# Kernel optimization log

Measured on AMD Instinct MI355X. Metric: run time of the kernel, lower is better.

The kernel has to match this reference:

```python
import jax, jax.numpy as jnp
import numpy as np

E = 1024  # hidden_size
H = 16    # num_heads
D = E // H  # head_dim
LN_EPS = 1e-5


def setup_inputs() -> dict:
    key = jax.random.key(0)
    ks = jax.random.split(key, 7)
    B, S = 4, 2048
    scale = 1.0 / np.sqrt(E)
    return {
        "txt_emb": jax.random.normal(ks[0], (B, S, E), dtype=jnp.float32),
        "in_proj_w": jax.random.normal(ks[1], (3 * E, E), dtype=jnp.float32) * scale,
        "in_proj_b": jnp.zeros((3 * E,), dtype=jnp.float32),
        "out_proj_w": jax.random.normal(ks[2], (E, E), dtype=jnp.float32) * scale,
        "out_proj_b": jnp.zeros((E,), dtype=jnp.float32),
        "ln_gamma": jnp.ones((E,), dtype=jnp.float32),
        "ln_beta": jnp.zeros((E,), dtype=jnp.float32),
    }


def _layer_norm(x, gamma, beta):
    mu = jnp.mean(x, axis=-1, keepdims=True)
    var = jnp.var(x, axis=-1, keepdims=True)
    return (x - mu) * jax.lax.rsqrt(var + LN_EPS) * gamma + beta


def reference(txt_emb, in_proj_w, in_proj_b, out_proj_w, out_proj_b, ln_gamma, ln_beta):
    B, S, _ = txt_emb.shape
    # joint QKV projection (torch nn.MultiheadAttention semantics: x @ W.T + b)
    qkv = jnp.einsum('bse,fe->bsf', txt_emb, in_proj_w) + in_proj_b  # [B,S,3E]
    q, k, v = jnp.split(qkv, 3, axis=-1)
    # [B,H,S,D]
    q = q.reshape(B, S, H, D).transpose(0, 2, 1, 3)
    k = k.reshape(B, S, H, D).transpose(0, 2, 1, 3)
    v = v.reshape(B, S, H, D).transpose(0, 2, 1, 3)
    scores = jnp.einsum('bhqd,bhkd->bhqk', q, k) / np.sqrt(D)  # [B,H,S,S]
    causal = jnp.tril(jnp.ones((S, S), dtype=bool))
    scores = jnp.where(causal, scores, jnp.float32(-jnp.inf))
    attn = jax.nn.softmax(scores, axis=-1)
    ctx = jnp.einsum('bhqk,bhkd->bhqd', attn, v)  # [B,H,S,D]
    ctx = ctx.transpose(0, 2, 1, 3).reshape(B, S, E)
    attn_out = jnp.einsum('bse,fe->bsf', ctx, out_proj_w) + out_proj_b
    return _layer_norm(txt_emb + attn_out, ln_gamma, ln_beta)
```

## Files before the change

kernel.cpp:

```cpp
#include <hip/hip_runtime.h>
#include <hip/hip_bf16.h>
#include <stdint.h>

#define B_   4
#define S_   2048
#define E_   1024
#define H_   16
#define D_   64
#define M_   (B_ * S_)
#define E3_  (3 * E_)

#define QSCALE 0.18033688011112042f

typedef __bf16 bf16_t;
typedef bf16_t bf16x8 __attribute__((ext_vector_type(8)));
typedef float  f32x4  __attribute__((ext_vector_type(4)));
typedef float  f32x16 __attribute__((ext_vector_type(16)));

__device__ __forceinline__ ushort f2bf(float f) {
  union { float f; uint32_t u; } v; v.f = f;
  uint32_t r = v.u + 0x7fffu + ((v.u >> 16) & 1u);
  return (ushort)(r >> 16);
}

__device__ __forceinline__ unsigned cvtpk(float lo, float hi_) {
  unsigned d;
  asm("v_cvt_pk_bf16_f32 %0, %1, %2" : "=v"(d) : "v"(lo), "v"(hi_));
  return d;
}

__device__ __forceinline__ void gload_lds16(const void* g, void* l) {
  __builtin_amdgcn_global_load_lds((const __attribute__((address_space(1))) void*)g,
                                   (__attribute__((address_space(3))) void*)l,
                                   16, 0, 0);
}

__global__ __launch_bounds__(256) void cvt_f32_bf16(const float* __restrict__ in,
                                                    ushort* __restrict__ out, int n4,
                                                    int scale_row4, float scale) {
  int i = blockIdx.x * blockDim.x + threadIdx.x;
  if (i < n4) {
    float4 v = reinterpret_cast<const float4*>(in)[i];
    if (i < scale_row4) { v.x *= scale; v.y *= scale; v.z *= scale; v.w *= scale; }
    ushort4 o;
    o.x = f2bf(v.x); o.y = f2bf(v.y); o.z = f2bf(v.z); o.w = f2bf(v.w);
    reinterpret_cast<ushort4*>(out)[i] = o;
  }
}

__global__ __launch_bounds__(512) void gemm_qkv_8ph(const ushort* __restrict__ A,
                                                    const ushort* __restrict__ Bt,
                                                    const float* __restrict__ bias,
                                                    ushort* __restrict__ qkout,
                                                    ushort* __restrict__ vTout) {
  __shared__ __align__(16) char lds[3][49152];

  const int tid = threadIdx.x;
  const int lane = tid & 63, wid = tid >> 6;
  const int wr = wid >> 2, wc = wid & 3;

  const int b0 = blockIdx.x;
  const int nb = (b0 & 7) * 96 + (b0 >> 3);
  const int bm = (nb / 12) * 128;
  const int bn = (nb % 12) * 256;

  const int l8 = lane >> 3;
  const int sw = (lane & 7) ^ l8;
  const ushort* aS = A  + (size_t)(bm + wid * 16 + l8) * 1024 + sw * 8;
  const ushort* bS = Bt + (size_t)(bn + wid * 32 + l8) * 1024 + sw * 8;

#define STAGE_A(T, BUF, J) \
  gload_lds16(aS + (size_t)(T) * 64 + (J) * 8 * 1024, (void*)((BUF) + (wid * 2 + (J)) * 1024))
#define STAGE_B(T, BUF, J) \
  gload_lds16(bS + (size_t)(T) * 64 + (J) * 8 * 1024, (void*)((BUF) + 16384 + (wid * 4 + (J)) * 1024))

  const int lr15 = lane & 15;
  const int ksub = lane >> 4;
  const int slot0 = ((ksub + 0) ^ (lr15 & 7)) * 16;
  const int slot1 = ((ksub + 4) ^ (lr15 & 7)) * 16;
  const int arow_b = (wr * 64 + lr15) * 128;
  const int brow_b = (wc * 64 + lr15) * 128;

#define LDA_ALL(BUF)                                                              \
  do {                                                                            \
    _Pragma("unroll")                                                             \
    for (int m = 0; m < 4; ++m) {                                                 \
      af[m][0] = *(const bf16x8*)((BUF) + arow_b + m * 2048 + slot0);             \
      af[m][1] = *(const bf16x8*)((BUF) + arow_b + m * 2048 + slot1);             \
    }                                                                             \
  } while (0)
#define LDB2(BUF, NB)                                                             \
  do {                                                                            \
    _Pragma("unroll")                                                             \
    for (int n = 0; n < 2; ++n) {                                                 \
      bfr[n][0] = *(const bf16x8*)((BUF) + 16384 + brow_b + ((NB) + n) * 2048 + slot0); \
      bfr[n][1] = *(const bf16x8*)((BUF) + 16384 + brow_b + ((NB) + n) * 2048 + slot1); \
    }                                                                             \
  } while (0)
#define MFMA16(NB)                                                                \
  do {                                                                            \
    __builtin_amdgcn_s_setprio(1);                                                \
    _Pragma("unroll")                                                             \
    for (int m = 0; m < 4; ++m)                                                   \
      _Pragma("unroll")                                                           \
      for (int n = 0; n < 2; ++n)                                                 \
        _Pragma("unroll")                                                         \
        for (int kh = 0; kh < 2; ++kh)                                            \
          acc[m][(NB) + n] = __builtin_amdgcn_mfma_f32_16x16x32_bf16(             \
              af[m][kh], bfr[n][kh], acc[m][(NB) + n], 0, 0, 0);                  \
    __builtin_amdgcn_s_setprio(0);                                                \
  } while (0)

  f32x4 acc[4][4] = {};
  bf16x8 af[4][2], bfr[2][2];

  char* buf0 = &lds[0][0];
  char* buf1 = &lds[1][0];
  char* buf2 = &lds[2][0];

  STAGE_A(0, buf0, 0); STAGE_A(0, buf0, 1);
  STAGE_B(0, buf0, 0); STAGE_B(0, buf0, 1); STAGE_B(0, buf0, 2); STAGE_B(0, buf0, 3);
  STAGE_A(1, buf1, 0); STAGE_A(1, buf1, 1);
  STAGE_B(1, buf1, 0); STAGE_B(1, buf1, 1); STAGE_B(1, buf1, 2); STAGE_B(1, buf1, 3);
  asm volatile("s_waitcnt vmcnt(6)" ::: "memory");
  __builtin_amdgcn_s_barrier();
  __builtin_amdgcn_sched_barrier(0);

  for (int t = 0; t < 16; ++t) {
    if (t < 14) { STAGE_A(t + 2, buf2, 0); STAGE_A(t + 2, buf2, 1); STAGE_B(t + 2, buf2, 0); }
    LDA_ALL(buf0);
    LDB2(buf0, 0);
    __builtin_amdgcn_s_barrier();
    asm volatile("s_waitcnt lgkmcnt(0)" ::: "memory");
    __builtin_amdgcn_sched_barrier(0);
    MFMA16(0);
    __builtin_amdgcn_s_barrier();
    __builtin_amdgcn_sched_barrier(0);
    if (t < 14) { STAGE_B(t + 2, buf2, 1); STAGE_B(t + 2, buf2, 2); STAGE_B(t + 2, buf2, 3); }
    LDB2(buf0, 2);
    __builtin_amdgcn_s_barrier();
    asm volatile("s_waitcnt lgkmcnt(0)" ::: "memory");
    __builtin_amdgcn_sched_barrier(0);
    MFMA16(2);
    if (t < 14) asm volatile("s_waitcnt vmcnt(6)" ::: "memory");
    else if (t == 14) asm volatile("s_waitcnt vmcnt(0)" ::: "memory");
    __builtin_amdgcn_s_barrier();
    __builtin_amdgcn_sched_barrier(0);
    char* tmp = buf0; buf0 = buf1; buf1 = buf2; buf2 = tmp;
  }

#pragma unroll
  for (int m = 0; m < 4; ++m) {
#pragma unroll
    for (int n = 0; n < 4; ++n) {
      const int col = bn + wc * 64 + n * 16 + lr15;
      float bv = bias[col];
      if (col < 1024) bv *= QSCALE;
      const int row0 = bm + wr * 64 + m * 16 + ksub * 4;
      if (col < 2048) {
#pragma unroll
        for (int r = 0; r < 4; ++r)
          qkout[(size_t)(row0 + r) * 2048 + col] = f2bf(acc[m][n][r] + bv);
      } else {
        ushort4 vv;
        vv.x = f2bf(acc[m][n][0] + bv);
        vv.y = f2bf(acc[m][n][1] + bv);
        vv.z = f2bf(acc[m][n][2] + bv);
        vv.w = f2bf(acc[m][n][3] + bv);
        const size_t vidx = ((size_t)((row0 >> 11) * 1024 + (col - 2048))) * 2048 + (row0 & 2047);
        *reinterpret_cast<ushort4*>(&vTout[vidx]) = vv;
      }
    }
  }
#undef STAGE_A
#undef STAGE_B
#undef LDA_ALL
#undef LDB2
#undef MFMA16
}

__global__ __launch_bounds__(256) void gemm_bt0(const ushort* __restrict__ A,
                                                const ushort* __restrict__ Bt,
                                                const float* __restrict__ bias,
                                                float* __restrict__ out0,
                                                int Mdim, int Ndim, int K) {
  __shared__ __align__(16) ushort As[128 * 32];
  __shared__ __align__(16) ushort Bs[128 * 32];

  const int tid  = threadIdx.x;
  const int lane = tid & 63, wid = tid >> 6;
  const int wr = wid >> 1, wc = wid & 1;

  const int nx = gridDim.x;
  const int nwg = nx * gridDim.y;
  const int b0 = blockIdx.y * nx + blockIdx.x;
  const int nb = (b0 & 7) * (nwg >> 3) + (b0 >> 3);
  const int bm = (nb / nx) * 128, bn = (nb % nx) * 128;

  const int lrow = lane & 15, lk8 = (lane >> 4) * 8, lg4 = (lane >> 4) * 4;
  const int srow = tid >> 2;
  const int skk  = (tid & 3) * 8;

  f32x4 acc[4][4] = {};

  for (int k0 = 0; k0 < K; k0 += 32) {
#pragma unroll
    for (int j = 0; j < 2; ++j) {
      const ushort* ga = A  + (size_t)(bm + j * 64 + srow) * K + k0 + skk;
      const ushort* gb = Bt + (size_t)(bn + j * 64 + srow) * K + k0 + skk;
      gload_lds16(ga, (void*)&As[(j * 256 + wid * 64) * 8]);
      gload_lds16(gb, (void*)&Bs[(j * 256 + wid * 64) * 8]);
    }
    __syncthreads();

    bf16x8 af[4], bfv[4];
#pragma unroll
    for (int rb = 0; rb < 4; ++rb)
      af[rb] = *reinterpret_cast<const bf16x8*>(&As[(wr * 64 + rb * 16 + lrow) * 32 + lk8]);
#pragma unroll
    for (int cb = 0; cb < 4; ++cb)
      bfv[cb] = *reinterpret_cast<const bf16x8*>(&Bs[(wc * 64 + cb * 16 + lrow) * 32 + lk8]);
#pragma unroll
    for (int rb = 0; rb < 4; ++rb)
#pragma unroll
      for (int cb = 0; cb < 4; ++cb)
        acc[rb][cb] = __builtin_amdgcn_mfma_f32_16x16x32_bf16(af[rb], bfv[cb], acc[rb][cb], 0, 0, 0);
    __syncthreads();
  }

#pragma unroll
  for (int rb = 0; rb < 4; ++rb) {
#pragma unroll
    for (int cb = 0; cb < 4; ++cb) {
      const int col = bn + wc * 64 + cb * 16 + lrow;
      const float bv = bias[col];
      const int row0 = bm + wr * 64 + rb * 16 + lg4;
#pragma unroll
      for (int r = 0; r < 4; ++r)
        out0[(size_t)(row0 + r) * Ndim + col] = acc[rb][cb][r] + bv;
    }
  }
}

__global__ __launch_bounds__(512) void attn_causal(const ushort* __restrict__ qk,
                                                   const ushort* __restrict__ vT,
                                                   ushort* __restrict__ ctx) {
  __shared__ __align__(16) char lds[2][16384];

  const int tid = threadIdx.x;
  const int w = tid >> 6, lane = tid & 63;
  const int l31 = lane & 31, hi = lane >> 5;

  const int bid = blockIdx.x;
  const int bh = (bid & 7) * 8 + ((bid >> 3) & 7);
  const int g6 = bid >> 6;
  const int qb = (g6 < 4) ? (7 - g6) : (g6 - 4);
  const int b = bh >> 4, h = bh & 15;
  const int qbase = qb * 256;
  const int tmax = 4 * qb + 3;
  const int qw = qbase + w * 32;
  const int q_g = qw + l31;
  const int my_tmax = (qw + 31) >> 6;

  const ushort* qrow = qk + (size_t)(b * S_ + q_g) * 2048 + h * 64;
  bf16x8 qf[4];
#pragma unroll
  for (int st = 0; st < 4; ++st)
    qf[st] = *reinterpret_cast<const bf16x8*>(qrow + st * 16 + hi * 8);

  const int srow = tid >> 3;
  const int swz  = ((tid & 7) * 16) ^ ((srow & 7) << 4);
  const char* kbase = (const char*)qk + ((size_t)(b * S_ + srow) * 2048 + 1024 + h * 64) * 2 + swz;
  const char* vbase = (const char*)vT + ((size_t)(bh * 64 + srow) * 2048) * 2 + swz;

  f32x16 Ot0 = {}, Ot1 = {};
  float m_r = -__builtin_inff(), l_r = 0.f;

  const int kswz = ((l31 & 7) << 4);

#define STAGE(T, BUFI)                                                              \
  do {                                                                              \
    gload_lds16(kbase + (size_t)(T) * (64 * 2048 * 2), &lds[BUFI][w * 1024]);       \
    gload_lds16(vbase + (size_t)(T) * 128,             &lds[BUFI][8192 + w * 1024]);\
  } while (0)

  STAGE(0, 0);
  for (int t = 0; t <= tmax; ++t) {
    const int bufi = t & 1;
    if (t < tmax) {
      STAGE(t + 1, bufi ^ 1);
      asm volatile("s_waitcnt vmcnt(2)" ::: "memory");
    } else {
      asm volatile("s_waitcnt vmcnt(0)" ::: "memory");
    }
    __builtin_amdgcn_s_barrier();
    __builtin_amdgcn_sched_barrier(0);

    if (t <= my_tmax) {
      const char* Kt = &lds[bufi][0];
      const char* Vp = &lds[bufi][8192];

      f32x16 T0 = {}, T1 = {};
#pragma unroll
      for (int st = 0; st < 4; ++st) {
        const int cb = (st * 32 + hi * 16) ^ kswz;
        bf16x8 k0 = *(const bf16x8*)(Kt + l31 * 128 + cb);
        bf16x8 k1 = *(const bf16x8*)(Kt + (32 + l31) * 128 + cb);
        T0 = __builtin_amdgcn_mfma_f32_32x32x16_bf16(k0, qf[st], T0, 0, 0, 0);
        T1 = __builtin_amdgcn_mfma_f32_32x32x16_bf16(k1, qf[st], T1, 0, 0, 0);
      }

      float p[32];
      const bool needmask = (t * 64 + 63) > qw;
      const int kvb = t * 64 + 4 * hi;
#pragma unroll
      for (int g = 0; g < 4; ++g) {
#pragma unroll
        for (int j = 0; j < 4; ++j) {
          float v0 = T0[4 * g + j], v1 = T1[4 * g + j];
          if (needmask) {
            const int kv0 = kvb + 8 * g + j;
            v0 = (kv0      <= q_g) ? v0 : -__builtin_inff();
            v1 = (kv0 + 32 <= q_g) ? v1 : -__builtin_inff();
          }
          p[4 * g + j] = v0;
          p[16 + 4 * g + j] = v1;
        }
      }
      float pmax = p[0];
#pragma unroll
      for (int i = 1; i < 31; i += 2) pmax = fmaxf(fmaxf(pmax, p[i]), p[i + 1]);
      pmax = fmaxf(pmax, p[31]);
      pmax = fmaxf(pmax, __shfl_xor(pmax, 32));

      if (!__all(pmax - m_r <= 8.f)) {
        const float mn = fmaxf(m_r, pmax);
        const float sc = exp2f(m_r - mn);
        m_r = mn;
        l_r *= sc;
#pragma unroll
        for (int i = 0; i < 16; ++i) { Ot0[i] *= sc; Ot1[i] *= sc; }
      }
      float sum = 0.f;
#pragma unroll
      for (int i = 0; i < 32; ++i) { p[i] = exp2f(p[i] - m_r); sum += p[i]; }
      sum += __shfl_xor(sum, 32);
      l_r += sum;

#pragma unroll
      for (int ks = 0; ks < 4; ++ks) {
        const unsigned a = cvtpk(p[8 * ks + 0], p[8 * ks + 1]);
        const unsigned bq = cvtpk(p[8 * ks + 2], p[8 * ks + 3]);
        const unsigned c = cvtpk(p[8 * ks + 4], p[8 * ks + 5]);
        const unsigned d = cvtpk(p[8 * ks + 6], p[8 * ks + 7]);
        const unsigned x = hi ? a : c;
        const unsigned y = hi ? bq : d;
        const unsigned xp = (unsigned)__shfl_xor((int)x, 32);
        const unsigned yp = (unsigned)__shfl_xor((int)y, 32);
        union { unsigned u[4]; bf16x8 v; } pa;
        pa.u[0] = hi ? xp : a;
        pa.u[1] = hi ? yp : bq;
        pa.u[2] = hi ? c : xp;
        pa.u[3] = hi ? d : yp;
        const int cb = (ks * 32 + hi * 16) ^ kswz;
        bf16x8 v0 = *(const bf16x8*)(Vp + l31 * 128 + cb);
        bf16x8 v1 = *(const bf16x8*)(Vp + (32 + l31) * 128 + cb);
        Ot0 = __builtin_amdgcn_mfma_f32_32x32x16_bf16(v0, pa.v, Ot0, 0, 0, 0);
        Ot1 = __builtin_amdgcn_mfma_f32_32x32x16_bf16(v1, pa.v, Ot1, 0, 0, 0);
      }
    }
    __builtin_amdgcn_s_barrier();
    __builtin_amdgcn_sched_barrier(0);
  }

  const float inv = 1.0f / l_r;
  ushort* crow = ctx + (size_t)(b * S_ + q_g) * 1024 + h * 64;
#pragma unroll
  for (int g = 0; g < 4; ++g) {
#pragma unroll
    for (int jp = 0; jp < 2; ++jp) {
      const int d0 = 2 * jp + 8 * g + 4 * hi;
      const int r = 4 * g + 2 * jp;
      *(unsigned*)(crow + d0)      = cvtpk(Ot0[r] * inv, Ot0[r + 1] * inv);
      *(unsigned*)(crow + 32 + d0) = cvtpk(Ot1[r] * inv, Ot1[r + 1] * inv);
    }
  }
#undef STAGE
}

__global__ __launch_bounds__(256) void resid_ln(const float* __restrict__ x,
                                                const float* __restrict__ ao,
                                                const float* __restrict__ gamma,
                                                const float* __restrict__ beta,
                                                float* __restrict__ out) {
  const int row = blockIdx.x;
  const int tid = threadIdx.x;
  const size_t base = (size_t)row * E_;

  float4 xv = reinterpret_cast<const float4*>(x + base)[tid];
  float4 av = reinterpret_cast<const float4*>(ao + base)[tid];
  const float v0 = xv.x + av.x, v1 = xv.y + av.y, v2 = xv.z + av.z, v3 = xv.w + av.w;
  float s  = v0 + v1 + v2 + v3;
  float s2 = v0 * v0 + v1 * v1 + v2 * v2 + v3 * v3;
#pragma unroll
  for (int off = 32; off >= 1; off >>= 1) {
    s  += __shfl_xor(s, off);
    s2 += __shfl_xor(s2, off);
  }
  __shared__ float red[8];
  const int wid = tid >> 6, lane = tid & 63;
  if (lane == 0) { red[wid] = s; red[4 + wid] = s2; }
  __syncthreads();
  s  = red[0] + red[1] + red[2] + red[3];
  s2 = red[4] + red[5] + red[6] + red[7];
  const float mu  = s * (1.f / E_);
  const float var = s2 * (1.f / E_) - mu * mu;
  const float rsd = rsqrtf(var + 1e-5f);

  float4 gv = reinterpret_cast<const float4*>(gamma)[tid];
  float4 bv = reinterpret_cast<const float4*>(beta)[tid];
  float4 ov;
  ov.x = (v0 - mu) * rsd * gv.x + bv.x;
  ov.y = (v1 - mu) * rsd * gv.y + bv.y;
  ov.z = (v2 - mu) * rsd * gv.z + bv.z;
  ov.w = (v3 - mu) * rsd * gv.w + bv.w;
  reinterpret_cast<float4*>(out + base)[tid] = ov;
}

extern "C" void kernel_launch(void* const* d_in, const int* in_sizes, int n_in,
                              void* d_out, int out_size, void* d_ws, size_t ws_size,
                              hipStream_t stream) {
  (void)in_sizes; (void)n_in; (void)out_size; (void)ws_size;
  const float* x     = (const float*)d_in[0];
  const float* w_in  = (const float*)d_in[1];
  const float* b_in  = (const float*)d_in[2];
  const float* w_out = (const float*)d_in[3];
  const float* b_out = (const float*)d_in[4];
  const float* gamma = (const float*)d_in[5];
  const float* beta  = (const float*)d_in[6];
  float* out = (float*)d_out;

  char* ws = (char*)d_ws;
  ushort* xb    = (ushort*)(ws);
  ushort* winb  = (ushort*)(ws + 16777216);
  ushort* woutb = (ushort*)(ws + 23068672);
  ushort* qkb   = (ushort*)(ws + 25165824);
  ushort* vTb   = (ushort*)(ws + 58720256);
  ushort* ctxb  = (ushort*)(ws + 75497472);
  float*  ao    = (float*)(ws + 92274688);

  cvt_f32_bf16<<<dim3((M_ * E_) / 4 / 256), 256, 0, stream>>>(x, xb, (M_ * E_) / 4, 0, 1.f);
  cvt_f32_bf16<<<dim3((E3_ * E_) / 4 / 256), 256, 0, stream>>>(w_in, winb, (E3_ * E_) / 4,
                                                               (E_ * E_) / 4, QSCALE);
  cvt_f32_bf16<<<dim3((E_ * E_) / 4 / 256), 256, 0, stream>>>(w_out, woutb, (E_ * E_) / 4, 0, 1.f);

  gemm_qkv_8ph<<<dim3(768), 512, 0, stream>>>(xb, winb, b_in, qkb, vTb);
  attn_causal<<<dim3(512), 512, 0, stream>>>(qkb, vTb, ctxb);
  gemm_bt0<<<dim3(E_ / 128, M_ / 128), 256, 0, stream>>>(ctxb, woutb, b_out, ao, M_, E_, E_);
  resid_ln<<<dim3(M_), 256, 0, stream>>>(x, ao, gamma, beta, out);
}
```

Measured before the change: 212.0 us.

## Pipeline output projection GEMM with triple-buffered LDS and rebalance causal attention rows

Replaces the simple single-buffered output-projection GEMM with a 512-thread, 128x256-tile kernel. It uses a three-stage LDS ring with staggered async global-to-LDS loads, swizzled LDS layout and MFMA priority hints, modeled on the existing QKV GEMM. This is meant to hide global load latency and cut barrier stalls. Separately, the causal attention kernel now assigns each workgroup interleaved query strips across the whole sequence, so every block does a similar amount of causal work instead of whole 256-row query blocks of very different length. This adds a larger LDS footprint per block, fewer GEMM workgroups, and longer KV loops per attention block.

```diff
diff --git a/kernel.cpp b/kernel.cpp
--- a/kernel.cpp
+++ b/kernel.cpp
@@ -179,67 +179,123 @@
 #undef MFMA16
 }
 
-__global__ __launch_bounds__(256) void gemm_bt0(const ushort* __restrict__ A,
-                                                const ushort* __restrict__ Bt,
-                                                const float* __restrict__ bias,
-                                                float* __restrict__ out0,
-                                                int Mdim, int Ndim, int K) {
-  __shared__ __align__(16) ushort As[128 * 32];
-  __shared__ __align__(16) ushort Bs[128 * 32];
-
-  const int tid  = threadIdx.x;
+__global__ __launch_bounds__(512) void gemm_out_8ph(const ushort* __restrict__ A,
+                                                    const ushort* __restrict__ Bt,
+                                                    const float* __restrict__ bias,
+                                                    float* __restrict__ out0) {
+  __shared__ __align__(16) char lds[3][49152];
+
+  const int tid = threadIdx.x;
   const int lane = tid & 63, wid = tid >> 6;
-  const int wr = wid >> 1, wc = wid & 1;
-
-  const int nx = gridDim.x;
-  const int nwg = nx * gridDim.y;
-  const int b0 = blockIdx.y * nx + blockIdx.x;
-  const int nb = (b0 & 7) * (nwg >> 3) + (b0 >> 3);
-  const int bm = (nb / nx) * 128, bn = (nb % nx) * 128;
-
-  const int lrow = lane & 15, lk8 = (lane >> 4) * 8, lg4 = (lane >> 4) * 4;
-  const int srow = tid >> 2;
-  const int skk  = (tid & 3) * 8;
+  const int wr = wid >> 2, wc = wid & 3;
+
+  const int b0 = blockIdx.x;
+  const int nb = (b0 & 7) * 32 + (b0 >> 3);
+  const int bm = (nb >> 2) * 128;
+  const int bn = (nb & 3) * 256;
+
+  const int l8 = lane >> 3;
+  const int sw = (lane & 7) ^ l8;
+  const ushort* aS = A  + (size_t)(bm + wid * 16 + l8) * 1024 + sw * 8;
+  const ushort* bS = Bt + (size_t)(bn + wid * 32 + l8) * 1024 + sw * 8;
+
+#define STAGE_A(T, BUF, J) \
+  gload_lds16(aS + (size_t)(T) * 64 + (J) * 8 * 1024, (void*)((BUF) + (wid * 2 + (J)) * 1024))
+#define STAGE_B(T, BUF, J) \
+  gload_lds16(bS + (size_t)(T) * 64 + (J) * 8 * 1024, (void*)((BUF) + 16384 + (wid * 4 + (J)) * 1024))
+
+  const int lr15 = lane & 15;
+  const int ksub = lane >> 4;
+  const int slot0 = ((ksub + 0) ^ (lr15 & 7)) * 16;
+  const int slot1 = ((ksub + 4) ^ (lr15 & 7)) * 16;
+  const int arow_b = (wr * 64 + lr15) * 128;
+  const int brow_b = (wc * 64 + lr15) * 128;
+
+#define LDA_ALL(BUF)                                                              \
+  do {                                                                            \
+    _Pragma("unroll")                                                             \
+    for (int m = 0; m < 4; ++m) {                                                 \
+      af[m][0] = *(const bf16x8*)((BUF) + arow_b + m * 2048 + slot0);             \
+      af[m][1] = *(const bf16x8*)((BUF) + arow_b + m * 2048 + slot1);             \
+    }                                                                             \
+  } while (0)
+#define LDB2(BUF, NB)                                                             \
+  do {                                                                            \
+    _Pragma("unroll")                                                             \
+    for (int n = 0; n < 2; ++n) {                                                 \
+      bfr[n][0] = *(const bf16x8*)((BUF) + 16384 + brow_b + ((NB) + n) * 2048 + slot0); \
+      bfr[n][1] = *(const bf16x8*)((BUF) + 16384 + brow_b + ((NB) + n) * 2048 + slot1); \
+    }                                                                             \
+  } while (0)
+#define MFMA16(NB)                                                                \
+  do {                                                                            \
+    __builtin_amdgcn_s_setprio(1);                                                \
+    _Pragma("unroll")                                                             \
+    for (int m = 0; m < 4; ++m)                                                   \
+      _Pragma("unroll")                                                           \
+      for (int n = 0; n < 2; ++n)                                                 \
+        _Pragma("unroll")                                                         \
+        for (int kh = 0; kh < 2; ++kh)                                            \
+          acc[m][(NB) + n] = __builtin_amdgcn_mfma_f32_16x16x32_bf16(             \
+              af[m][kh], bfr[n][kh], acc[m][(NB) + n], 0, 0, 0);                  \
+    __builtin_amdgcn_s_setprio(0);                                                \
+  } while (0)
 
   f32x4 acc[4][4] = {};
-
-  for (int k0 = 0; k0 < K; k0 += 32) {
-#pragma unroll
-    for (int j = 0; j < 2; ++j) {
-      const ushort* ga = A  + (size_t)(bm + j * 64 + srow) * K + k0 + skk;
-      const ushort* gb = Bt + (size_t)(bn + j * 64 + srow) * K + k0 + skk;
-      gload_lds16(ga, (void*)&As[(j * 256 + wid * 64) * 8]);
-      gload_lds16(gb, (void*)&Bs[(j * 256 + wid * 64) * 8]);
+  bf16x8 af[4][2], bfr[2][2];
+
+  char* buf0 = &lds[0][0];
+  char* buf1 = &lds[1][0];
+  char* buf2 = &lds[2][0];
+
+  STAGE_A(0, buf0, 0); STAGE_A(0, buf0, 1);
+  STAGE_B(0, buf0, 0); STAGE_B(0, buf0, 1); STAGE_B(0, buf0, 2); STAGE_B(0, buf0, 3);
+  STAGE_A(1, buf1, 0); STAGE_A(1, buf1, 1);
+  STAGE_B(1, buf1, 0); STAGE_B(1, buf1, 1); STAGE_B(1, buf1, 2); STAGE_B(1, buf1, 3);
+  asm volatile("s_waitcnt vmcnt(6)" ::: "memory");
+  __builtin_amdgcn_s_barrier();
+  __builtin_amdgcn_sched_barrier(0);
+
+  for (int t = 0; t < 16; ++t) {
+    if (t < 14) { STAGE_A(t + 2, buf2, 0); STAGE_A(t + 2, buf2, 1); STAGE_B(t + 2, buf2, 0); }
+    LDA_ALL(buf0);
+    LDB2(buf0, 0);
+    __builtin_amdgcn_s_barrier();
+    asm volatile("s_waitcnt lgkmcnt(0)" ::: "memory");
+    __builtin_amdgcn_sched_barrier(0);
+    MFMA16(0);
+    __builtin_amdgcn_s_barrier();
+    __builtin_amdgcn_sched_barrier(0);
+    if (t < 14) { STAGE_B(t + 2, buf2, 1); STAGE_B(t + 2, buf2, 2); STAGE_B(t + 2, buf2, 3); }
+    LDB2(buf0, 2);
+    __builtin_amdgcn_s_barrier();
+    asm volatile("s_waitcnt lgkmcnt(0)" ::: "memory");
+    __builtin_amdgcn_sched_barrier(0);
+    MFMA16(2);
+    if (t < 14) asm volatile("s_waitcnt vmcnt(6)" ::: "memory");
+    else if (t == 14) asm volatile("s_waitcnt vmcnt(0)" ::: "memory");
+    __builtin_amdgcn_s_barrier();
+    __builtin_amdgcn_sched_barrier(0);
+    char* tmp = buf0; buf0 = buf1; buf1 = buf2; buf2 = tmp;
+  }
+
+#pragma unroll
+  for (int m = 0; m < 4; ++m) {
+#pragma unroll
+    for (int n = 0; n < 4; ++n) {
+      const int col = bn + wc * 64 + n * 16 + lr15;
+      const float bv = bias[col];
+      const int row0 = bm + wr * 64 + m * 16 + ksub * 4;
+#pragma unroll
+      for (int r = 0; r < 4; ++r)
+        out0[(size_t)(row0 + r) * 1024 + col] = acc[m][n][r] + bv;
     }
-    __syncthreads();
-
-    bf16x8 af[4], bfv[4];
-#pragma unroll
-    for (int rb = 0; rb < 4; ++rb)
-      af[rb] = *reinterpret_cast<const bf16x8*>(&As[(wr * 64 + rb * 16 + lrow) * 32 + lk8]);
-#pragma unroll
-    for (int cb = 0; cb < 4; ++cb)
-      bfv[cb] = *reinterpret_cast<const bf16x8*>(&Bs[(wc * 64 + cb * 16 + lrow) * 32 + lk8]);
-#pragma unroll
-    for (int rb = 0; rb < 4; ++rb)
-#pragma unroll
-      for (int cb = 0; cb < 4; ++cb)
-        acc[rb][cb] = __builtin_amdgcn_mfma_f32_16x16x32_bf16(af[rb], bfv[cb], acc[rb][cb], 0, 0, 0);
-    __syncthreads();
-  }
-
-#pragma unroll
-  for (int rb = 0; rb < 4; ++rb) {
-#pragma unroll
-    for (int cb = 0; cb < 4; ++cb) {
-      const int col = bn + wc * 64 + cb * 16 + lrow;
-      const float bv = bias[col];
-      const int row0 = bm + wr * 64 + rb * 16 + lg4;
-#pragma unroll
-      for (int r = 0; r < 4; ++r)
-        out0[(size_t)(row0 + r) * Ndim + col] = acc[rb][cb][r] + bv;
-    }
-  }
+  }
+#undef STAGE_A
+#undef STAGE_B
+#undef LDA_ALL
+#undef LDB2
+#undef MFMA16
 }
 
 __global__ __launch_bounds__(512) void attn_causal(const ushort* __restrict__ qk,
@@ -253,14 +309,12 @@
 
   const int bid = blockIdx.x;
   const int bh = (bid & 7) * 8 + ((bid >> 3) & 7);
-  const int g6 = bid >> 6;
-  const int qb = (g6 < 4) ? (7 - g6) : (g6 - 4);
+  const int j = bid >> 6;
   const int b = bh >> 4, h = bh & 15;
-  const int qbase = qb * 256;
-  const int tmax = 4 * qb + 3;
-  const int qw = qbase + w * 32;
+  const int qw = w * 256 + j * 32;
   const int q_g = qw + l31;
   const int my_tmax = (qw + 31) >> 6;
+  const int tmax = 28 + (j >> 1);
 
   const ushort* qrow = qk + (size_t)(b * S_ + q_g) * 2048 + h * 64;
   bf16x8 qf[4];
@@ -316,15 +370,15 @@
 #pragma unroll
       for (int g = 0; g < 4; ++g) {
 #pragma unroll
-        for (int j = 0; j < 4; ++j) {
-          float v0 = T0[4 * g + j], v1 = T1[4 * g + j];
+        for (int jj = 0; jj < 4; ++jj) {
+          float v0 = T0[4 * g + jj], v1 = T1[4 * g + jj];
           if (needmask) {
-            const int kv0 = kvb + 8 * g + j;
+            const int kv0 = kvb + 8 * g + jj;
             v0 = (kv0      <= q_g) ? v0 : -__builtin_inff();
             v1 = (kv0 + 32 <= q_g) ? v1 : -__builtin_inff();
           }
-          p[4 * g + j] = v0;
-          p[16 + 4 * g + j] = v1;
+          p[4 * g + jj] = v0;
+          p[16 + 4 * g + jj] = v1;
         }
       }
       float pmax = p[0];
@@ -456,6 +510,6 @@
 
   gemm_qkv_8ph<<<dim3(768), 512, 0, stream>>>(xb, winb, b_in, qkb, vTb);
   attn_causal<<<dim3(512), 512, 0, stream>>>(qkb, vTb, ctxb);
-  gemm_bt0<<<dim3(E_ / 128, M_ / 128), 256, 0, stream>>>(ctxb, woutb, b_out, ao, M_, E_, E_);
+  gemm_out_8ph<<<dim3(256), 512, 0, stream>>>(ctxb, woutb, b_out, ao);
   resid_ln<<<dim3(M_), 256, 0, stream>>>(x, ao, gamma, beta, out);
 }
```

Result: slower. 221.3 us (+4.4%).
